# Optimization experiments

Hardware: AMD Instinct MI355X
Metric: run time of the kernel (lower is better)

The kernel has to match this reference:

```python
import jax, jax.numpy as jnp
import numpy as np

B, C, D = 16384, 512, 512
EXT = 2
H = C * EXT
TAU = 1.0          # temperature_train
STEP = 0.05        # langevin_step_size
NOISE = 0.1        # langevin_noise
STEPS = 32         # langevin_steps


def setup_inputs() -> dict:
    key = jax.random.key(0)
    ks = jax.random.split(key, 8)
    s_in = 1.0 / np.sqrt(D)
    s_h = 1.0 / np.sqrt(H)
    return {
        'x': jax.random.normal(ks[0], (B, D), jnp.float32),
        'vanilla_components': jnp.abs(jax.random.normal(ks[1], (C, D), jnp.float32) * 0.1),
        'e_sp': jax.random.normal(ks[2], (C * D,), jnp.float32) * 0.1,
        'W1e': jax.random.normal(ks[3], (D, H), jnp.float32) * s_in,
        'b1e': jnp.zeros((H,), jnp.float32),
        'W2e': jax.random.normal(ks[4], (H, C), jnp.float32) * s_h,
        'b2e': jnp.zeros((C,), jnp.float32),
        'W1r': jax.random.normal(ks[5], (D, H), jnp.float32) * s_in,
        'b1r': jnp.zeros((H,), jnp.float32),
        'W2r': jax.random.normal(ks[6], (H, C), jnp.float32) * s_h,
        'b2r': jnp.zeros((C,), jnp.float32),
    }


def _langevin_gate(e, key):
    """Langevin MCMC on latent u with quadratic energy E(u)=0.5||u||^2 + <e,u>.
    Returns selection probability sigmoid(-u/tau)."""
    def step(u, k):
        grad = u + e  # dE/du
        u = u - STEP * grad + NOISE * jax.random.normal(k, u.shape, u.dtype)
        return u, None
    u, _ = jax.lax.scan(step, jnp.zeros_like(e), jax.random.split(key, STEPS))
    return jax.nn.sigmoid(-u / TAU)


def reference(x, vanilla_components, e_sp, W1e, b1e, W2e, b2e, W1r, b1r, W2r, b2r):
    k1, k2 = jax.random.split(jax.random.key(42))
    # non-negative components
    comps = jnp.abs(vanilla_components)  # [C, D]
    # fixed energy-based sparsity mask over component entries
    p_sp = _langevin_gate(e_sp, k1).reshape(C, D)
    comps = comps * p_sp
    # dynamic per-sample component selection energies via MLP
    h = jax.nn.relu(x @ W1e + b1e)          # [B, H]
    e_dyn = h @ W2e + b2e                   # [B, C]
    gate = _langevin_gate(e_dyn, k2)        # [B, C] soft gates (train mode)
    hr = jax.nn.relu(x @ W1r + b1r)         # [B, H]
    conc = (hr @ W2r + b2r) * gate          # [B, C]
    # aggregate: (concentration * components).sum over components -> [B, D]
    return conc @ comps
```

## Files before the change

### kernel.cpp

```cpp
#include <hip/hip_runtime.h>
#include <hip/hip_bf16.h>
#include <stdint.h>

#define Bn 16384
#define Cn 512
#define Dn 512
#define Hn 1024

#define A32 0.80628851f

typedef __attribute__((ext_vector_type(8))) short bf16x8;
typedef __attribute__((ext_vector_type(4))) float f32x4;
typedef __attribute__((ext_vector_type(2))) float f32x2;

__device__ __forceinline__ ushort f2bf(float f) {
  uint32_t u = __float_as_uint(f);
  return (ushort)((u + 0x7fffu + ((u >> 16) & 1u)) >> 16);
}
__device__ __forceinline__ float b2f(ushort u) {
  return __uint_as_float((uint32_t)u << 16);
}

constexpr uint32_t crotl(uint32_t v, int s) {
  return (v << s) | (v >> (32 - s));
}
struct TFOut { uint32_t w0, w1; };
constexpr TFOut ctf(uint32_t k0, uint32_t k1, uint32_t x0, uint32_t x1) {
  const uint32_t ks[3] = {k0, k1, k0 ^ k1 ^ 0x1BD11BDAu};
  const int rot[8] = {13, 15, 26, 6, 17, 29, 16, 24};
  uint32_t a = x0 + k0, b = x1 + k1;
  for (int g = 0; g < 5; ++g) {
    for (int i = 0; i < 4; ++i) {
      int r = rot[(g & 1) * 4 + i];
      a += b; b = crotl(b, r); b ^= a;
    }
    a += ks[(g + 1) % 3];
    b += ks[(g + 2) % 3] + (uint32_t)(g + 1);
  }
  return {a, b};
}
struct KeySched { uint32_t s[64]; uint32_t d[64]; };
constexpr KeySched make_keys() {
  KeySched K{};
  TFOut k1 = ctf(0u, 42u, 0u, 0u);
  TFOut k2 = ctf(0u, 42u, 0u, 1u);
  for (uint32_t t = 0; t < 32; ++t) {
    TFOut ws = ctf(k1.w0, k1.w1, 0u, t);
    K.s[2 * t] = ws.w0; K.s[2 * t + 1] = ws.w1;
    TFOut wd = ctf(k2.w0, k2.w1, 0u, t);
    K.d[2 * t] = wd.w0; K.d[2 * t + 1] = wd.w1;
  }
  return K;
}
constexpr KeySched KS = make_keys();

__device__ __forceinline__ uint32_t rotl32(uint32_t v, int s) {
  return __builtin_rotateleft32(v, (uint32_t)s);
}
__device__ __forceinline__ uint32_t tf_xor(uint32_t K0, uint32_t K1,
                                           uint32_t KX, uint32_t j) {
  uint32_t a = K0, b = K1 + j;
#define TR(r) { a += b; b = rotl32(b, (r)); b ^= a; }
  TR(13) TR(15) TR(26) TR(6)   a += K1; b += KX + 1u;
  TR(17) TR(29) TR(16) TR(24)  a += KX; b += K0 + 2u;
  TR(13) TR(15) TR(26) TR(6)   a += K0; b += K1 + 3u;
  TR(17) TR(29) TR(16) TR(24)  a += K1; b += KX + 4u;
  TR(13) TR(15) TR(26) TR(6)   a += KX; b += K0 + 5u;
#undef TR
  return a ^ b;
}

__device__ __forceinline__ float bits_to_normal(uint32_t bits) {
  float f = __uint_as_float((bits >> 9) | 0x3f800000u) - 1.0f;
  float x = f * 2.0f - 0x1.fffffep-1f;
  float w = -__logf(1.0f - x * x);
  float p;
  if (w < 5.0f) {
    w -= 2.5f;
    p =            2.81022636e-08f;
    p = fmaf(p, w, 3.43273939e-07f);
    p = fmaf(p, w, -3.5233877e-06f);
    p = fmaf(p, w, -4.39150654e-06f);
    p = fmaf(p, w, 0.00021858087f);
    p = fmaf(p, w, -0.00125372503f);
    p = fmaf(p, w, -0.00417768164f);
    p = fmaf(p, w, 0.246640727f);
    p = fmaf(p, w, 1.50140941f);
  } else {
    w = sqrtf(w) - 3.0f;
    p =            -0.000200214257f;
    p = fmaf(p, w, 0.000100950558f);
    p = fmaf(p, w, 0.00134934322f);
    p = fmaf(p, w, -0.00367342844f);
    p = fmaf(p, w, 0.00573950773f);
    p = fmaf(p, w, -0.0076224613f);
    p = fmaf(p, w, 0.00943887047f);
    p = fmaf(p, w, 1.00167406f);
    p = fmaf(p, w, 2.83297682f);
  }
  return 0x1.6a09e6p+0f * (p * x);
}

__global__ __launch_bounds__(256) void k_z(ushort* __restrict__ Z) {
  const uint32_t j0 = (blockIdx.x * 256u + threadIdx.x) * 2u;
  const uint32_t j1 = j0 + 1u;
  float z0 = 0.0f, z1 = 0.0f;
#pragma unroll
  for (int t = 0; t < 32; ++t) {
    const uint32_t K0 = KS.d[2 * t], K1 = KS.d[2 * t + 1];
    const uint32_t KX = K0 ^ K1 ^ 0x1BD11BDAu;
    uint32_t a0 = K0, b0 = K1 + j0;
    uint32_t a1 = K0, b1 = K1 + j1;
#define R2(r)                                                  \
    a0 += b0; a1 += b1;                                        \
    b0 = rotl32(b0, (r)); b1 = rotl32(b1, (r));                \
    b0 ^= a0; b1 ^= a1;
#define I2(p, q) a0 += (p); a1 += (p); b0 += (q); b1 += (q);
    R2(13) R2(15) R2(26) R2(6)  I2(K1, KX + 1u)
    R2(17) R2(29) R2(16) R2(24) I2(KX, K0 + 2u)
    R2(13) R2(15) R2(26) R2(6)  I2(K0, K1 + 3u)
    R2(17) R2(29) R2(16) R2(24) I2(K1, KX + 4u)
    R2(13) R2(15) R2(26) R2(6)  I2(KX, K0 + 5u)
#undef R2
#undef I2
    uint32_t s0 = a0 ^ b0, s1 = a1 ^ b1;
    float f0 = __uint_as_float((s0 >> 9) | 0x3f800000u) - 1.0f;
    float f1 = __uint_as_float((s1 >> 9) | 0x3f800000u) - 1.0f;
    float x0 = f0 * 2.0f - 0x1.fffffep-1f;
    float x1 = f1 * 2.0f - 0x1.fffffep-1f;
    float w0 = fminf(-__logf(fmaf(-x0, x0, 1.0f)), 5.0f) - 2.5f;
    float w1 = fminf(-__logf(fmaf(-x1, x1, 1.0f)), 5.0f) - 2.5f;
    f32x2 X = {x0, x1}, W = {w0, w1};
    f32x2 P = {2.81022636e-08f, 2.81022636e-08f};
    P = __builtin_elementwise_fma(P, W, (f32x2){3.43273939e-07f, 3.43273939e-07f});
    P = __builtin_elementwise_fma(P, W, (f32x2){-3.5233877e-06f, -3.5233877e-06f});
    P = __builtin_elementwise_fma(P, W, (f32x2){-4.39150654e-06f, -4.39150654e-06f});
    P = __builtin_elementwise_fma(P, W, (f32x2){0.00021858087f, 0.00021858087f});
    P = __builtin_elementwise_fma(P, W, (f32x2){-0.00125372503f, -0.00125372503f});
    P = __builtin_elementwise_fma(P, W, (f32x2){-0.00417768164f, -0.00417768164f});
    P = __builtin_elementwise_fma(P, W, (f32x2){0.246640727f, 0.246640727f});
    P = __builtin_elementwise_fma(P, W, (f32x2){1.50140941f, 1.50140941f});
    f32x2 Q = (P * X) * (f32x2){0.14142135f, 0.14142135f};
    z0 = fmaf(0.95f, z0, Q.x);
    z1 = fmaf(0.95f, z1, Q.y);
  }
  *(ushort2*)(Z + j0) = make_ushort2(f2bf(z0), f2bf(z1));
}

__device__ __forceinline__ void transpose_tile(
    const float* __restrict__ in, ushort* __restrict__ out,
    int N, int K, int tIdx, float T[32][33]) {
  const int ntn = N / 32;
  const int tk = tIdx / ntn, tn = tIdx % ntn;
  const int tx = threadIdx.x & 31, ty = threadIdx.x >> 5;
  const int k0 = tk * 32, n0 = tn * 32;
#pragma unroll
  for (int r = 0; r < 32; r += 8)
    T[ty + r][tx] = in[(size_t)(k0 + ty + r) * N + n0 + tx];
  __syncthreads();
#pragma unroll
  for (int r = 0; r < 32; r += 8)
    out[(size_t)(n0 + ty + r) * K + k0 + tx] = f2bf(T[tx][ty + r]);
}

__device__ __forceinline__ void smask_block(
    const float* __restrict__ vc, const float* __restrict__ e_sp,
    ushort* __restrict__ compsT, int g) {
  uint32_t jj = (uint32_t)g * 256 + threadIdx.x;
  uint32_t c = jj & (Cn - 1), d = jj >> 9;
  uint32_t ridx = c * Dn + d;
  float e = e_sp[ridx];
  float u = 0.0f;
#pragma unroll
  for (int t = 0; t < 32; ++t) {
    const uint32_t K0 = KS.s[2 * t], K1 = KS.s[2 * t + 1];
    uint32_t s = tf_xor(K0, K1, K0 ^ K1 ^ 0x1BD11BDAu, ridx);
    float n = bits_to_normal(s);
    u = (u - 0.05f * (u + e)) + 0.1f * n;
  }
  float gt = 1.0f / (1.0f + __expf(u));
  compsT[jj] = f2bf(fabsf(vc[ridx]) * gt);
}

__global__ __launch_bounds__(256) void k_prep(
    const float* __restrict__ x, ushort* __restrict__ x_bf,
    const float* __restrict__ W1e, ushort* __restrict__ W1eT,
    const float* __restrict__ W2e, ushort* __restrict__ W2eT,
    const float* __restrict__ W1r, ushort* __restrict__ W1rT,
    const float* __restrict__ W2r, ushort* __restrict__ W2rT,
    const float* __restrict__ vc, const float* __restrict__ e_sp,
    ushort* __restrict__ compsT) {
  __shared__ float T[32][33];
  const int pos = blockIdx.x;
  if (pos < 8192) {
    int i = (pos * 256 + threadIdx.x) * 4;
    float4 v = *(const float4*)(x + i);
    *(ushort4*)(x_bf + i) =
        make_ushort4(f2bf(v.x), f2bf(v.y), f2bf(v.z), f2bf(v.w));
  } else if (pos < 8704) {
    transpose_tile(W1e, W1eT, Hn, Dn, pos - 8192, T);
  } else if (pos < 9216) {
    transpose_tile(W2e, W2eT, Cn, Hn, pos - 8704, T);
  } else if (pos < 9728) {
    transpose_tile(W1r, W1rT, Hn, Dn, pos - 9216, T);
  } else if (pos < 10240) {
    transpose_tile(W2r, W2rT, Cn, Hn, pos - 9728, T);
  } else {
    smask_block(vc, e_sp, compsT, pos - 10240);
  }
}

__device__ __forceinline__ void gemm_tile_bf(
    const ushort* __restrict__ A, const ushort* __restrict__ WT,
    const float* __restrict__ bias, ushort* __restrict__ Out, int g,
    ushort As[128][40], ushort Bs[128][40]) {
  const int n0 = (g & 7) * 128, m0 = (g >> 3) * 128;
  const int t = threadIdx.x;
  const int srow = t >> 1, skb = (t & 1) << 4;
  const ushort* Ap = A  + (size_t)(m0 + srow) * Dn + skb;
  const ushort* Bp = WT + (size_t)(n0 + srow) * Dn + skb;
  const int wave = t >> 6, lane = t & 63;
  const int wm = (wave >> 1) << 6, wn = (wave & 1) << 6;
  const int quad = lane >> 4, l15 = lane & 15;

  f32x4 acc[4][4] = {};
  for (int k0 = 0; k0 < Dn; k0 += 32) {
    uint4 a0 = *(const uint4*)(Ap + k0);
    uint4 a1 = *(const uint4*)(Ap + k0 + 8);
    uint4 b0 = *(const uint4*)(Bp + k0);
    uint4 b1 = *(const uint4*)(Bp + k0 + 8);
    *(uint4*)&As[srow][skb] = a0; *(uint4*)&As[srow][skb + 8] = a1;
    *(uint4*)&Bs[srow][skb] = b0; *(uint4*)&Bs[srow][skb + 8] = b1;
    __syncthreads();
    bf16x8 af[4], bfr[4];
#pragma unroll
    for (int i = 0; i < 4; ++i) {
      af[i] = *(const bf16x8*)&As[wm + i * 16 + l15][quad * 8];
      bfr[i] = *(const bf16x8*)&Bs[wn + i * 16 + l15][quad * 8];
    }
#pragma unroll
    for (int i = 0; i < 4; ++i)
#pragma unroll
      for (int j = 0; j < 4; ++j)
        acc[i][j] = __builtin_amdgcn_mfma_f32_16x16x32_bf16(af[i], bfr[j],
                                                            acc[i][j], 0, 0, 0);
    __syncthreads();
  }
#pragma unroll
  for (int i = 0; i < 4; ++i)
#pragma unroll
    for (int j = 0; j < 4; ++j) {
      const int col = n0 + wn + j * 16 + l15;
      const float bv = bias[col];
#pragma unroll
      for (int r = 0; r < 4; ++r) {
        const int row = m0 + wm + i * 16 + quad * 4 + r;
        Out[(size_t)row * Hn + col] = f2bf(fmaxf(acc[i][j][r] + bv, 0.0f));
      }
    }
}

__global__ __launch_bounds__(256) void k_g13(
    const ushort* __restrict__ x_bf,
    const ushort* __restrict__ W1eT, const float* __restrict__ b1e,
    ushort* __restrict__ h,
    const ushort* __restrict__ W1rT, const float* __restrict__ b1r,
    ushort* __restrict__ hr) {
  __shared__ ushort As[128][40];
  __shared__ ushort Bs[128][40];
  const int pos = blockIdx.x;
  const int g = pos >> 1;
  if (pos & 1)
    gemm_tile_bf(x_bf, W1rT, b1r, hr, g, As, Bs);
  else
    gemm_tile_bf(x_bf, W1eT, b1e, h, g, As, Bs);
}

__global__ __launch_bounds__(256) void k_dgemm(
    const ushort* __restrict__ h, const ushort* __restrict__ W2eT,
    const float* __restrict__ b2e,
    const ushort* __restrict__ hr, const ushort* __restrict__ W2rT,
    const float* __restrict__ b2r,
    ushort* __restrict__ Zconc) {
  __shared__ ushort As[128][40];
  __shared__ ushort Bs[128][40];
  const int t = threadIdx.x;
  const int m0 = blockIdx.y * 128, n0 = blockIdx.x * 128;
  const int srow = t >> 1, skb = (t & 1) << 4;
  const int wave = t >> 6, lane = t & 63;
  const int wm = (wave >> 1) << 6, wn = (wave & 1) << 6;
  const int quad = lane >> 4, l15 = lane & 15;

  const ushort* Ap = h    + (size_t)(m0 + srow) * Hn + skb;
  const ushort* Bp = W2eT + (size_t)(n0 + srow) * Hn + skb;
  f32x4 acc[4][4] = {};
  for (int k0 = 0; k0 < Hn; k0 += 32) {
    uint4 a0 = *(const uint4*)(Ap + k0);
    uint4 a1 = *(const uint4*)(Ap + k0 + 8);
    uint4 b0 = *(const uint4*)(Bp + k0);
    uint4 b1 = *(const uint4*)(Bp + k0 + 8);
    *(uint4*)&As[srow][skb] = a0; *(uint4*)&As[srow][skb + 8] = a1;
    *(uint4*)&Bs[srow][skb] = b0; *(uint4*)&Bs[srow][skb + 8] = b1;
    __syncthreads();
    bf16x8 af[4], bfr[4];
#pragma unroll
    for (int i = 0; i < 4; ++i) {
      af[i] = *(const bf16x8*)&As[wm + i * 16 + l15][quad * 8];
      bfr[i] = *(const bf16x8*)&Bs[wn + i * 16 + l15][quad * 8];
    }
#pragma unroll
    for (int i = 0; i < 4; ++i)
#pragma unroll
      for (int j = 0; j < 4; ++j)
        acc[i][j] = __builtin_amdgcn_mfma_f32_16x16x32_bf16(af[i], bfr[j],
                                                            acc[i][j], 0, 0, 0);
    __syncthreads();
  }
  float g[4][4][4];
#pragma unroll
  for (int i = 0; i < 4; ++i)
#pragma unroll
    for (int j = 0; j < 4; ++j) {
      const int col = n0 + wn + j * 16 + l15;
      const float bv = b2e[col];
#pragma unroll
      for (int r = 0; r < 4; ++r) {
        const int row = m0 + wm + i * 16 + quad * 4 + r;
        float e = acc[i][j][r] + bv;
        float z = b2f(Zconc[(size_t)row * Cn + col]);
        g[i][j][r] = 1.0f / (1.0f + __expf(z - A32 * e));
        acc[i][j][r] = 0.0f;
      }
    }
  Ap = hr   + (size_t)(m0 + srow) * Hn + skb;
  Bp = W2rT + (size_t)(n0 + srow) * Hn + skb;
  for (int k0 = 0; k0 < Hn; k0 += 32) {
    uint4 a0 = *(const uint4*)(Ap + k0);
    uint4 a1 = *(const uint4*)(Ap + k0 + 8);
    uint4 b0 = *(const uint4*)(Bp + k0);
    uint4 b1 = *(const uint4*)(Bp + k0 + 8);
    __syncthreads();
    *(uint4*)&As[srow][skb] = a0; *(uint4*)&As[srow][skb + 8] = a1;
    *(uint4*)&Bs[srow][skb] = b0; *(uint4*)&Bs[srow][skb + 8] = b1;
    __syncthreads();
    bf16x8 af[4], bfr[4];
#pragma unroll
    for (int i = 0; i < 4; ++i) {
      af[i] = *(const bf16x8*)&As[wm + i * 16 + l15][quad * 8];
      bfr[i] = *(const bf16x8*)&Bs[wn + i * 16 + l15][quad * 8];
    }
#pragma unroll
    for (int i = 0; i < 4; ++i)
#pragma unroll
      for (int j = 0; j < 4; ++j)
        acc[i][j] = __builtin_amdgcn_mfma_f32_16x16x32_bf16(af[i], bfr[j],
                                                            acc[i][j], 0, 0, 0);
  }
#pragma unroll
  for (int i = 0; i < 4; ++i)
#pragma unroll
    for (int j = 0; j < 4; ++j) {
      const int col = n0 + wn + j * 16 + l15;
      const float bv = b2r[col];
#pragma unroll
      for (int r = 0; r < 4; ++r) {
        const int row = m0 + wm + i * 16 + quad * 4 + r;
        Zconc[(size_t)row * Cn + col] = f2bf((acc[i][j][r] + bv) * g[i][j][r]);
      }
    }
}

__global__ __launch_bounds__(256) void k_gemm_out(
    const ushort* __restrict__ A, const ushort* __restrict__ WT,
    float* __restrict__ Out) {
  __shared__ ushort As[128][40];
  __shared__ ushort Bs[128][40];
  const int t = threadIdx.x;
  const int m0 = blockIdx.y * 128, n0 = blockIdx.x * 128;
  const int srow = t >> 1, skb = (t & 1) << 4;
  const ushort* Ap = A  + (size_t)(m0 + srow) * Cn + skb;
  const ushort* Bp = WT + (size_t)(n0 + srow) * Cn + skb;
  const int wave = t >> 6, lane = t & 63;
  const int wm = (wave >> 1) << 6, wn = (wave & 1) << 6;
  const int quad = lane >> 4, l15 = lane & 15;

  f32x4 acc[4][4] = {};
  for (int k0 = 0; k0 < Cn; k0 += 32) {
    uint4 a0 = *(const uint4*)(Ap + k0);
    uint4 a1 = *(const uint4*)(Ap + k0 + 8);
    uint4 b0 = *(const uint4*)(Bp + k0);
    uint4 b1 = *(const uint4*)(Bp + k0 + 8);
    *(uint4*)&As[srow][skb] = a0; *(uint4*)&As[srow][skb + 8] = a1;
    *(uint4*)&Bs[srow][skb] = b0; *(uint4*)&Bs[srow][skb + 8] = b1;
    __syncthreads();
    bf16x8 af[4], bfr[4];
#pragma unroll
    for (int i = 0; i < 4; ++i) {
      af[i] = *(const bf16x8*)&As[wm + i * 16 + l15][quad * 8];
      bfr[i] = *(const bf16x8*)&Bs[wn + i * 16 + l15][quad * 8];
    }
#pragma unroll
    for (int i = 0; i < 4; ++i)
#pragma unroll
      for (int j = 0; j < 4; ++j)
        acc[i][j] = __builtin_amdgcn_mfma_f32_16x16x32_bf16(af[i], bfr[j],
                                                            acc[i][j], 0, 0, 0);
    __syncthreads();
  }
#pragma unroll
  for (int i = 0; i < 4; ++i)
#pragma unroll
    for (int j = 0; j < 4; ++j) {
      const int col = n0 + wn + j * 16 + l15;
#pragma unroll
      for (int r = 0; r < 4; ++r) {
        const int row = m0 + wm + i * 16 + quad * 4 + r;
        Out[(size_t)row * Dn + col] = acc[i][j][r];
      }
    }
}

extern "C" void kernel_launch(void* const* d_in, const int* in_sizes, int n_in,
                              void* d_out, int out_size, void* d_ws, size_t ws_size,
                              hipStream_t stream) {
  const float* x    = (const float*)d_in[0];
  const float* vc   = (const float*)d_in[1];
  const float* e_sp = (const float*)d_in[2];
  const float* W1e  = (const float*)d_in[3];
  const float* b1e  = (const float*)d_in[4];
  const float* W2e  = (const float*)d_in[5];
  const float* b2e  = (const float*)d_in[6];
  const float* W1r  = (const float*)d_in[7];
  const float* b1r  = (const float*)d_in[8];
  const float* W2r  = (const float*)d_in[9];
  const float* b2r  = (const float*)d_in[10];
  float* out = (float*)d_out;

  char* ws = (char*)d_ws;
  ushort* W1eT   = (ushort*)(ws + (1u << 12));
  ushort* W2eT   = (ushort*)(ws + (1u << 12) + (1u << 20));
  ushort* W1rT   = (ushort*)(ws + (1u << 12) + (2u << 20));
  ushort* W2rT   = (ushort*)(ws + (1u << 12) + (3u << 20));
  ushort* compsT = (ushort*)(ws + (1u << 12) + (4u << 20));
  ushort* Zdyn   = (ushort*)(ws + (8u << 20));
  ushort* h_bf   = (ushort*)(ws + (24u << 20));
  ushort* hr_bf  = (ushort*)(ws + (56u << 20));
  ushort* x_bf   = (ushort*)d_out;

  k_prep<<<11264, 256, 0, stream>>>(x, x_bf, W1e, W1eT, W2e, W2eT,
                                    W1r, W1rT, W2r, W2rT, vc, e_sp, compsT);
  k_z<<<16384, 256, 0, stream>>>(Zdyn);
  k_g13<<<2048, 256, 0, stream>>>(x_bf, W1eT, b1e, h_bf, W1rT, b1r, hr_bf);
  k_dgemm<<<dim3(Cn / 128, Bn / 128), 256, 0, stream>>>(
      h_bf, W2eT, b2e, hr_bf, W2rT, b2r, Zdyn);
  k_gemm_out<<<dim3(Dn / 128, Bn / 128), 256, 0, stream>>>(Zdyn, compsT, out);
}
```

Before: 835.6 us.

## Interleave Langevin noise blocks into GEMM kernels and split gate into separate pass

Removes the standalone k_z noise kernel and spreads its blocks across the prep, first-layer GEMM, and two split second-layer GEMM kernels, so the ALU-bound Threefry/erfinv work runs alongside MFMA-bound tiles. The fused gate dgemm is split into separate e and conc GEMMs that write fp32 to scratch, plus an elementwise gate kernel. Key tables move to __constant__ and the RNG loops are only partially unrolled. This costs extra fp32 traffic for e and conc and one more launch, and the interleaved block ratios must exactly cover all noise indices.

```diff
diff --git a/kernel.cpp b/kernel.cpp
--- a/kernel.cpp
+++ b/kernel.cpp
@@ -52,7 +52,7 @@
   }
   return K;
 }
-constexpr KeySched KS = make_keys();
+__constant__ KeySched KS = make_keys();
 
 __device__ __forceinline__ uint32_t rotl32(uint32_t v, int s) {
   return __builtin_rotateleft32(v, (uint32_t)s);
@@ -101,11 +101,11 @@
   return 0x1.6a09e6p+0f * (p * x);
 }
 
-__global__ __launch_bounds__(256) void k_z(ushort* __restrict__ Z) {
-  const uint32_t j0 = (blockIdx.x * 256u + threadIdx.x) * 2u;
+__device__ __forceinline__ void z_block(ushort* __restrict__ Z, uint32_t zidx) {
+  const uint32_t j0 = (zidx * 256u + threadIdx.x) * 2u;
   const uint32_t j1 = j0 + 1u;
   float z0 = 0.0f, z1 = 0.0f;
-#pragma unroll
+#pragma unroll 4
   for (int t = 0; t < 32; ++t) {
     const uint32_t K0 = KS.d[2 * t], K1 = KS.d[2 * t + 1];
     const uint32_t KX = K0 ^ K1 ^ 0x1BD11BDAu;
@@ -171,7 +171,7 @@
   uint32_t ridx = c * Dn + d;
   float e = e_sp[ridx];
   float u = 0.0f;
-#pragma unroll
+#pragma unroll 4
   for (int t = 0; t < 32; ++t) {
     const uint32_t K0 = KS.s[2 * t], K1 = KS.s[2 * t + 1];
     uint32_t s = tf_xor(K0, K1, K0 ^ K1 ^ 0x1BD11BDAu, ridx);
@@ -182,31 +182,36 @@
   compsT[jj] = f2bf(fabsf(vc[ridx]) * gt);
 }
 
-__global__ __launch_bounds__(256) void k_prep(
+__global__ __launch_bounds__(256) void k_prep_z(
     const float* __restrict__ x, ushort* __restrict__ x_bf,
     const float* __restrict__ W1e, ushort* __restrict__ W1eT,
     const float* __restrict__ W2e, ushort* __restrict__ W2eT,
     const float* __restrict__ W1r, ushort* __restrict__ W1rT,
     const float* __restrict__ W2r, ushort* __restrict__ W2rT,
     const float* __restrict__ vc, const float* __restrict__ e_sp,
-    ushort* __restrict__ compsT) {
+    ushort* __restrict__ compsT, ushort* __restrict__ Zd) {
   __shared__ float T[32][33];
   const int pos = blockIdx.x;
-  if (pos < 8192) {
-    int i = (pos * 256 + threadIdx.x) * 4;
+  if ((pos % 5) == 4) {
+    z_block(Zd, (uint32_t)(pos / 5));
+    return;
+  }
+  const int p = (pos / 5) * 4 + (pos % 5);
+  if (p < 8192) {
+    int i = (p * 256 + threadIdx.x) * 4;
     float4 v = *(const float4*)(x + i);
     *(ushort4*)(x_bf + i) =
         make_ushort4(f2bf(v.x), f2bf(v.y), f2bf(v.z), f2bf(v.w));
-  } else if (pos < 8704) {
-    transpose_tile(W1e, W1eT, Hn, Dn, pos - 8192, T);
-  } else if (pos < 9216) {
-    transpose_tile(W2e, W2eT, Cn, Hn, pos - 8704, T);
-  } else if (pos < 9728) {
-    transpose_tile(W1r, W1rT, Hn, Dn, pos - 9216, T);
-  } else if (pos < 10240) {
-    transpose_tile(W2r, W2rT, Cn, Hn, pos - 9728, T);
+  } else if (p < 8704) {
+    transpose_tile(W1e, W1eT, Hn, Dn, p - 8192, T);
+  } else if (p < 9216) {
+    transpose_tile(W2e, W2eT, Cn, Hn, p - 8704, T);
+  } else if (p < 9728) {
+    transpose_tile(W1r, W1rT, Hn, Dn, p - 9216, T);
+  } else if (p < 10240) {
+    transpose_tile(W2r, W2rT, Cn, Hn, p - 9728, T);
   } else {
-    smask_block(vc, e_sp, compsT, pos - 10240);
+    smask_block(vc, e_sp, compsT, p - 10240);
   }
 }
 
@@ -260,39 +265,39 @@
     }
 }
 
-__global__ __launch_bounds__(256) void k_g13(
+__global__ __launch_bounds__(256) void k_g13_z(
     const ushort* __restrict__ x_bf,
     const ushort* __restrict__ W1eT, const float* __restrict__ b1e,
     ushort* __restrict__ h,
     const ushort* __restrict__ W1rT, const float* __restrict__ b1r,
-    ushort* __restrict__ hr) {
+    ushort* __restrict__ hr, ushort* __restrict__ Zd) {
   __shared__ ushort As[128][40];
   __shared__ ushort Bs[128][40];
   const int pos = blockIdx.x;
-  const int g = pos >> 1;
-  if (pos & 1)
+  if (pos % 3) {
+    z_block(Zd, 2816u + (uint32_t)(pos / 3) * 2u + (uint32_t)(pos % 3) - 1u);
+    return;
+  }
+  const int gg = pos / 3;
+  const int g = gg >> 1;
+  if (gg & 1)
     gemm_tile_bf(x_bf, W1rT, b1r, hr, g, As, Bs);
   else
     gemm_tile_bf(x_bf, W1eT, b1e, h, g, As, Bs);
 }
 
-__global__ __launch_bounds__(256) void k_dgemm(
-    const ushort* __restrict__ h, const ushort* __restrict__ W2eT,
-    const float* __restrict__ b2e,
-    const ushort* __restrict__ hr, const ushort* __restrict__ W2rT,
-    const float* __restrict__ b2r,
-    ushort* __restrict__ Zconc) {
-  __shared__ ushort As[128][40];
-  __shared__ ushort Bs[128][40];
+__device__ __forceinline__ void gemm_tile_f32out(
+    const ushort* __restrict__ A, const ushort* __restrict__ WT,
+    const float* __restrict__ bias, float* __restrict__ Out,
+    int m0, int n0, ushort As[128][40], ushort Bs[128][40]) {
   const int t = threadIdx.x;
-  const int m0 = blockIdx.y * 128, n0 = blockIdx.x * 128;
   const int srow = t >> 1, skb = (t & 1) << 4;
+  const ushort* Ap = A  + (size_t)(m0 + srow) * Hn + skb;
+  const ushort* Bp = WT + (size_t)(n0 + srow) * Hn + skb;
   const int wave = t >> 6, lane = t & 63;
   const int wm = (wave >> 1) << 6, wn = (wave & 1) << 6;
   const int quad = lane >> 4, l15 = lane & 15;
 
-  const ushort* Ap = h    + (size_t)(m0 + srow) * Hn + skb;
-  const ushort* Bp = W2eT + (size_t)(n0 + srow) * Hn + skb;
   f32x4 acc[4][4] = {};
   for (int k0 = 0; k0 < Hn; k0 += 32) {
     uint4 a0 = *(const uint4*)(Ap + k0);
@@ -316,58 +321,76 @@
                                                             acc[i][j], 0, 0, 0);
     __syncthreads();
   }
-  float g[4][4][4];
 #pragma unroll
   for (int i = 0; i < 4; ++i)
 #pragma unroll
     for (int j = 0; j < 4; ++j) {
       const int col = n0 + wn + j * 16 + l15;
-      const float bv = b2e[col];
+      const float bv = bias[col];
 #pragma unroll
       for (int r = 0; r < 4; ++r) {
         const int row = m0 + wm + i * 16 + quad * 4 + r;
-        float e = acc[i][j][r] + bv;
-        float z = b2f(Zconc[(size_t)row * Cn + col]);
-        g[i][j][r] = 1.0f / (1.0f + __expf(z - A32 * e));
-        acc[i][j][r] = 0.0f;
+        Out[(size_t)row * Cn + col] = acc[i][j][r] + bv;
       }
     }
-  Ap = hr   + (size_t)(m0 + srow) * Hn + skb;
-  Bp = W2rT + (size_t)(n0 + srow) * Hn + skb;
-  for (int k0 = 0; k0 < Hn; k0 += 32) {
-    uint4 a0 = *(const uint4*)(Ap + k0);
-    uint4 a1 = *(const uint4*)(Ap + k0 + 8);
-    uint4 b0 = *(const uint4*)(Bp + k0);
-    uint4 b1 = *(const uint4*)(Bp + k0 + 8);
-    __syncthreads();
-    *(uint4*)&As[srow][skb] = a0; *(uint4*)&As[srow][skb + 8] = a1;
-    *(uint4*)&Bs[srow][skb] = b0; *(uint4*)&Bs[srow][skb + 8] = b1;
-    __syncthreads();
-    bf16x8 af[4], bfr[4];
-#pragma unroll
-    for (int i = 0; i < 4; ++i) {
-      af[i] = *(const bf16x8*)&As[wm + i * 16 + l15][quad * 8];
-      bfr[i] = *(const bf16x8*)&Bs[wn + i * 16 + l15][quad * 8];
-    }
-#pragma unroll
-    for (int i = 0; i < 4; ++i)
-#pragma unroll
-      for (int j = 0; j < 4; ++j)
-        acc[i][j] = __builtin_amdgcn_mfma_f32_16x16x32_bf16(af[i], bfr[j],
-                                                            acc[i][j], 0, 0, 0);
-  }
-#pragma unroll
-  for (int i = 0; i < 4; ++i)
-#pragma unroll
-    for (int j = 0; j < 4; ++j) {
-      const int col = n0 + wn + j * 16 + l15;
-      const float bv = b2r[col];
-#pragma unroll
-      for (int r = 0; r < 4; ++r) {
-        const int row = m0 + wm + i * 16 + quad * 4 + r;
-        Zconc[(size_t)row * Cn + col] = f2bf((acc[i][j][r] + bv) * g[i][j][r]);
-      }
-    }
+}
+
+__global__ __launch_bounds__(256) void k_e_z(
+    const ushort* __restrict__ h, const ushort* __restrict__ W2eT,
+    const float* __restrict__ b2e, float* __restrict__ e_out,
+    ushort* __restrict__ Zd) {
+  __shared__ ushort As[128][40];
+  __shared__ ushort Bs[128][40];
+  const int pos = blockIdx.x;
+  if ((pos % 10) == 0) {
+    const int tg = pos / 10;
+    gemm_tile_f32out(h, W2eT, b2e, e_out, (tg >> 2) * 128, (tg & 3) * 128,
+                     As, Bs);
+  } else {
+    z_block(Zd, 6912u + (uint32_t)(pos / 10) * 9u + (uint32_t)(pos % 10) - 1u);
+  }
+}
+
+__global__ __launch_bounds__(256) void k_r_z(
+    const ushort* __restrict__ hr, const ushort* __restrict__ W2rT,
+    const float* __restrict__ b2r, float* __restrict__ cr_out,
+    ushort* __restrict__ Zd) {
+  __shared__ ushort As[128][40];
+  __shared__ ushort Bs[128][40];
+  const int pos = blockIdx.x;
+  if (pos >= 5120) {
+    z_block(Zd, 16128u + (uint32_t)(pos - 5120));
+    return;
+  }
+  if ((pos % 10) == 0) {
+    const int tg = pos / 10;
+    gemm_tile_f32out(hr, W2rT, b2r, cr_out, (tg >> 2) * 128, (tg & 3) * 128,
+                     As, Bs);
+  } else {
+    z_block(Zd, 11520u + (uint32_t)(pos / 10) * 9u + (uint32_t)(pos % 10) - 1u);
+  }
+}
+
+__global__ __launch_bounds__(256) void k_gate(
+    const float* __restrict__ e, const float* __restrict__ cr,
+    ushort* __restrict__ Z) {
+  const size_t i = ((size_t)blockIdx.x * 256u + threadIdx.x) * 8u;
+  uint4 zv = *(const uint4*)(Z + i);
+  ushort zs[8];
+  *(uint4*)zs = zv;
+  float ee[8], cc[8];
+  *(float4*)(ee)     = *(const float4*)(e + i);
+  *(float4*)(ee + 4) = *(const float4*)(e + i + 4);
+  *(float4*)(cc)     = *(const float4*)(cr + i);
+  *(float4*)(cc + 4) = *(const float4*)(cr + i + 4);
+  ushort os[8];
+#pragma unroll
+  for (int k = 0; k < 8; ++k) {
+    float z = b2f(zs[k]);
+    float g = 1.0f / (1.0f + __expf(z - A32 * ee[k]));
+    os[k] = f2bf(cc[k] * g);
+  }
+  *(uint4*)(Z + i) = *(uint4*)os;
 }
 
 __global__ __launch_bounds__(256) void k_gemm_out(
@@ -445,13 +468,17 @@
   ushort* Zdyn   = (ushort*)(ws + (8u << 20));
   ushort* h_bf   = (ushort*)(ws + (24u << 20));
   ushort* hr_bf  = (ushort*)(ws + (56u << 20));
+  float*  cr_f32 = (float*)(ws + (24u << 20));
   ushort* x_bf   = (ushort*)d_out;
-
-  k_prep<<<11264, 256, 0, stream>>>(x, x_bf, W1e, W1eT, W2e, W2eT,
-                                    W1r, W1rT, W2r, W2rT, vc, e_sp, compsT);
-  k_z<<<16384, 256, 0, stream>>>(Zdyn);
-  k_g13<<<2048, 256, 0, stream>>>(x_bf, W1eT, b1e, h_bf, W1rT, b1r, hr_bf);
-  k_dgemm<<<dim3(Cn / 128, Bn / 128), 256, 0, stream>>>(
-      h_bf, W2eT, b2e, hr_bf, W2rT, b2r, Zdyn);
+  float*  e_f32  = (float*)d_out;
+
+  k_prep_z<<<14080, 256, 0, stream>>>(x, x_bf, W1e, W1eT, W2e, W2eT,
+                                      W1r, W1rT, W2r, W2rT, vc, e_sp, compsT,
+                                      Zdyn);
+  k_g13_z<<<6144, 256, 0, stream>>>(x_bf, W1eT, b1e, h_bf, W1rT, b1r, hr_bf,
+                                    Zdyn);
+  k_e_z<<<5120, 256, 0, stream>>>(h_bf, W2eT, b2e, e_f32, Zdyn);
+  k_r_z<<<5376, 256, 0, stream>>>(hr_bf, W2rT, b2r, cr_f32, Zdyn);
+  k_gate<<<4096, 256, 0, stream>>>(e_f32, cr_f32, Zdyn);
   k_gemm_out<<<dim3(Dn / 128, Bn / 128), 256, 0, stream>>>(Zdyn, compsT, out);
 }
```

Measured after the change: 800.4 us. 1.04x faster.
